# Kernel optimization log

Measured on AMD Instinct MI355X. Metric: run time of the kernel, lower is better.

Reference implementation:

```python
import jax, jax.numpy as jnp
import numpy as np

MIN_PS = 4
MAX_PS = 16


def _enforce(mb):
    # mb: (L,) bool candidate boundaries (merge_signal < 0.7-quantile)
    # Faithful re-implementation of _enforce_patch_size_constraints:
    # walk boundaries left->right, skip segments < MIN_PS (start not advanced),
    # accept otherwise, and insert ceil(ps/MAX_PS)-1 evenly spaced splits for
    # oversized segments. seq_len-1 is always appended as a candidate.
    L = mb.shape[0]
    pos = jnp.arange(L, dtype=jnp.int32)
    cand = mb | (pos == L - 1)

    def fwd_step(start, inp):
        p, is_c = inp
        ps = p - start
        acc = is_c & (ps >= MIN_PS)
        k = jnp.where(acc, (ps + MAX_PS - 1) // MAX_PS, jnp.int32(1))
        sz = jnp.maximum(jnp.where(acc, ps // k, jnp.int32(1)), 1)
        new_start = jnp.where(acc, p, start)
        return new_start, (acc, start, sz, k)

    _, (acc, seg_start, sz, k) = jax.lax.scan(fwd_step, jnp.int32(0), (pos, cand))

    # Reverse scan: propagate each accepted boundary's (start, split_size, num_splits)
    # back to the interior positions of its segment so splits can be placed in parallel.
    def rev_step(carry, inp):
        a, s, z, kk = inp
        cs, cz, ck, cv = carry
        out = (cs, cz, ck, cv)
        ncarry = (jnp.where(a, s, cs), jnp.where(a, z, cz), jnp.where(a, kk, ck), cv | a)
        return ncarry, out

    init = (jnp.int32(0), jnp.int32(1), jnp.int32(1), jnp.bool_(False))
    _, (fs, fz, fk, fv) = jax.lax.scan(rev_step, init, (acc, seg_start, sz, k), reverse=True)
    r = pos - fs
    j = r // fz
    split = fv & (r > 0) & (r % fz == 0) & (j >= 1) & (j <= fk - 1)
    return acc | split


def reference(x, attention_mask, W1, b1, W2, b2, Wc, bc, Wb1, bb1, Wb2, bb2):
    B, L, D = x.shape
    # content scorer: Linear -> ReLU -> Linear -> Sigmoid
    content = jax.nn.sigmoid(jax.nn.relu(x @ W1 + b1) @ W2 + b2)[..., 0]  # (B, L)
    # grouped Conv1d(d, d//2, k=3, pad=1, groups=d//4)
    xc = jnp.transpose(x, (0, 2, 1))  # (B, D, L)
    pf = jax.lax.conv_general_dilated(xc, Wc, (1,), ((1, 1),),
                                      feature_group_count=D // 4,
                                      dimension_numbers=('NCH', 'OIH', 'NCH'))
    pf = jnp.transpose(pf + bc[None, :, None], (0, 2, 1))  # (B, L, D//2)
    comb = jnp.concatenate([x, pf], axis=-1)
    bscore = jax.nn.sigmoid(jax.nn.relu(comb @ Wb1 + bb1) @ Wb2 + bb2)[..., 0]  # (B, L)
    signal = content * (1.0 - bscore) * attention_mask
    thr = jnp.quantile(signal, 0.7, axis=1, keepdims=True)
    mb = signal < thr
    new_b = jax.vmap(_enforce)(mb)  # (B, L) bool, new_b[:,0] is always False

    # segment id per token = inclusive cumsum of boundaries
    seg = jnp.cumsum(new_b.astype(jnp.int32), axis=1)
    seg_flat = (seg + jnp.arange(B, dtype=jnp.int32)[:, None] * L).reshape(-1)
    NS = B * L
    xm = x * attention_mask[..., None]
    e = jnp.sum(xm * xm, axis=-1).reshape(-1)  # softmax logits = ||token||^2
    m = jax.ops.segment_max(e, seg_flat, num_segments=NS)
    w = jnp.exp(e - m[seg_flat])
    denom = jax.ops.segment_sum(w, seg_flat, num_segments=NS)
    wn = w / denom[seg_flat]
    merged = jax.ops.segment_sum(xm.reshape(-1, D) * wn[:, None], seg_flat,
                                 num_segments=NS).reshape(B, L, D)
    # segment_boundaries: 1 for every segment except the first, zero padding
    n_last = seg[:, -1]
    p = jnp.arange(L)
    seg_bounds = ((p[None, :] >= 1) & (p[None, :] <= n_last[:, None])).astype(jnp.float32)
    return merged, seg_bounds


def setup_inputs() -> dict:
    key = jax.random.key(0)
    B, L, D = 4, 8192, 512
    ks = jax.random.split(key, 8)
    s = 0.02
    return {
        'x': jax.random.normal(ks[0], (B, L, D), jnp.float32),
        'attention_mask': jnp.ones((B, L), jnp.float32),
        'W1': jax.random.normal(ks[1], (D, D // 4), jnp.float32) * s,
        'b1': jnp.zeros((D // 4,), jnp.float32),
        'W2': jax.random.normal(ks[2], (D // 4, 1), jnp.float32) * s,
        'b2': jnp.zeros((1,), jnp.float32),
        'Wc': jax.random.normal(ks[3], (D // 2, 4, 3), jnp.float32) * s,
        'bc': jnp.zeros((D // 2,), jnp.float32),
        'Wb1': jax.random.normal(ks[4], (D + D // 2, D // 4), jnp.float32) * s,
        'bb1': jnp.zeros((D // 4,), jnp.float32),
        'Wb2': jax.random.normal(ks[5], (D // 4, 1), jnp.float32) * s,
        'bb2': jnp.zeros((1,), jnp.float32),
    }
```

## Files before the change

### kernel.cpp

```cpp
#include <hip/hip_runtime.h>
#include <math.h>

#define B_  4
#define L_  8192
#define D_  512
#define BL_ (B_*L_)
#define TOK 32
#define XS  36
#define KC  32
#define NCH (D_/KC)

__global__ __launch_bounds__(256, 4) void k_signal(
    const float* __restrict__ x, const float* __restrict__ mask,
    const float* __restrict__ W1, const float* __restrict__ b1,
    const float* __restrict__ W2, const float* __restrict__ b2,
    const float* __restrict__ Wc, const float* __restrict__ bc,
    const float* __restrict__ Wb1, const float* __restrict__ bb1,
    const float* __restrict__ Wb2, const float* __restrict__ bb2,
    float* __restrict__ signal, float* __restrict__ e)
{
  __shared__ float xt[KC][XS];
  __shared__ float pf[16][XS];

  const int t   = threadIdx.x;
  const int blk = blockIdx.x;
  const int b   = blk >> 8;
  const int l0  = (blk & 255) * TOK;
  const float* xb = x + (size_t)b * L_ * D_;

  const int jq = t & 31, tw = t >> 5;
  const int j0 = jq << 2, tok0 = tw << 2;

  const int stok = t >> 3, skk = t & 7;
  const int oo_c  = t >> 4;
  const int tokq  = t & 15;
  const int cb_c  = (oo_c >> 1) << 2;
  const int tok0c = tokq << 1;

  float a1[4][4], a2[4][4];
#pragma unroll
  for (int i = 0; i < 4; ++i)
#pragma unroll
    for (int j = 0; j < 4; ++j) { a1[i][j] = 0.f; a2[i][j] = 0.f; }
  float esacc = 0.f;

  for (int c = 0; c < NCH; ++c) {
    const int kc = c << 5;
    __syncthreads();

    {
      const float4 v = *reinterpret_cast<const float4*>(
          xb + (size_t)(l0 + stok) * D_ + kc + (skk << 2));
      esacc = fmaf(v.x, v.x, esacc); esacc = fmaf(v.y, v.y, esacc);
      esacc = fmaf(v.z, v.z, esacc); esacc = fmaf(v.w, v.w, esacc);
      const int r = skk << 2;
      xt[r + 0][stok] = v.x; xt[r + 1][stok] = v.y;
      xt[r + 2][stok] = v.z; xt[r + 3][stok] = v.w;
    }
    if (t < 16) {
      const int hh = t >> 3, kk = t & 7;
      const int l = hh ? (l0 + TOK) : (l0 - 1);
      float4 v = make_float4(0.f, 0.f, 0.f, 0.f);
      if (l >= 0 && l < L_)
        v = *reinterpret_cast<const float4*>(xb + (size_t)l * D_ + kc + (kk << 2));
      const int r = kk << 2, col = TOK + hh;
      xt[r + 0][col] = v.x; xt[r + 1][col] = v.y;
      xt[r + 2][col] = v.z; xt[r + 3][col] = v.w;
    }
    __syncthreads();

    {
      const int o = (c << 4) + oo_c;
      const float* wcp = Wc + o * 12;
      const float bco = bc[o];
      float acc0 = bco, acc1 = bco;
      const int tm1 = (tok0c == 0) ? TOK : tok0c - 1;
      const int tp2 = (tok0c == TOK - 2) ? TOK + 1 : tok0c + 2;
#pragma unroll
      for (int i = 0; i < 4; ++i) {
        const float w0 = wcp[i * 3 + 0], w1 = wcp[i * 3 + 1], w2 = wcp[i * 3 + 2];
        const float* row = &xt[cb_c + i][0];
        const float v0 = row[tm1], v1 = row[tok0c], v2 = row[tok0c + 1],
                    v3 = row[tp2];
        acc0 = fmaf(v2, w2, fmaf(v1, w1, fmaf(v0, w0, acc0)));
        acc1 = fmaf(v3, w2, fmaf(v2, w1, fmaf(v1, w0, acc1)));
      }
      pf[oo_c][tok0c]     = acc0;
      pf[oo_c][tok0c + 1] = acc1;
    }

    {
      const float* w1p = W1  + (size_t)kc * 128 + j0;
      const float* wbp = Wb1 + (size_t)kc * 128 + j0;
#pragma unroll 2
      for (int k = 0; k < KC; ++k) {
        const float4 w1 = *reinterpret_cast<const float4*>(w1p + (size_t)k * 128);
        const float4 wb = *reinterpret_cast<const float4*>(wbp + (size_t)k * 128);
        const float4 xv4 = *reinterpret_cast<const float4*>(&xt[k][tok0]);
        const float xv[4] = {xv4.x, xv4.y, xv4.z, xv4.w};
#pragma unroll
        for (int i = 0; i < 4; ++i) {
          a1[i][0] = fmaf(xv[i], w1.x, a1[i][0]);
          a1[i][1] = fmaf(xv[i], w1.y, a1[i][1]);
          a1[i][2] = fmaf(xv[i], w1.z, a1[i][2]);
          a1[i][3] = fmaf(xv[i], w1.w, a1[i][3]);
          a2[i][0] = fmaf(xv[i], wb.x, a2[i][0]);
          a2[i][1] = fmaf(xv[i], wb.y, a2[i][1]);
          a2[i][2] = fmaf(xv[i], wb.z, a2[i][2]);
          a2[i][3] = fmaf(xv[i], wb.w, a2[i][3]);
        }
      }
    }
    __syncthreads();

    {
      const float* wpp = Wb1 + (size_t)(512 + (c << 4)) * 128 + j0;
#pragma unroll 2
      for (int oo = 0; oo < 16; ++oo) {
        const float4 wp = *reinterpret_cast<const float4*>(wpp + (size_t)oo * 128);
        const float4 pv4 = *reinterpret_cast<const float4*>(&pf[oo][tok0]);
        const float pv[4] = {pv4.x, pv4.y, pv4.z, pv4.w};
#pragma unroll
        for (int i = 0; i < 4; ++i) {
          a2[i][0] = fmaf(pv[i], wp.x, a2[i][0]);
          a2[i][1] = fmaf(pv[i], wp.y, a2[i][1]);
          a2[i][2] = fmaf(pv[i], wp.z, a2[i][2]);
          a2[i][3] = fmaf(pv[i], wp.w, a2[i][3]);
        }
      }
    }
  }

  {
    float b1v[4], w2v[4], bbv[4], wv2[4];
#pragma unroll
    for (int jj = 0; jj < 4; ++jj) {
      b1v[jj] = b1[j0 + jj];  w2v[jj] = W2[j0 + jj];
      bbv[jj] = bb1[j0 + jj]; wv2[jj] = Wb2[j0 + jj];
    }
    const float bias2 = b2[0], biasb2 = bb2[0];
#pragma unroll
    for (int i = 0; i < 4; ++i) {
      float p1 = 0.f, p2 = 0.f;
#pragma unroll
      for (int jj = 0; jj < 4; ++jj) {
        const float h1 = a1[i][jj] + b1v[jj];
        if (h1 > 0.f) p1 = fmaf(h1, w2v[jj], p1);
        const float h2 = a2[i][jj] + bbv[jj];
        if (h2 > 0.f) p2 = fmaf(h2, wv2[jj], p2);
      }
#pragma unroll
      for (int off = 1; off < 32; off <<= 1) {
        p1 += __shfl_xor(p1, off, 64);
        p2 += __shfl_xor(p2, off, 64);
      }
      if (jq == 0) {
        const int gi = b * L_ + l0 + tok0 + i;
        const float content = 1.f / (1.f + expf(-(p1 + bias2)));
        const float bscore  = 1.f / (1.f + expf(-(p2 + biasb2)));
        signal[gi] = content * (1.f - bscore) * mask[gi];
      }
    }
  }

  {
    float es = esacc;
    es += __shfl_xor(es, 1, 64);
    es += __shfl_xor(es, 2, 64);
    es += __shfl_xor(es, 4, 64);
    if ((t & 7) == 0) {
      const int gi = b * L_ + l0 + stok;
      const float m = mask[gi];
      e[gi] = m * m * es;
    }
  }
}

__device__ __forceinline__ int chain_sim(unsigned long long w, int from) {
  int last = -1;
  while (from < 64) {
    const unsigned long long m = w & (~0ull << from);
    if (m == 0ull) break;
    const int p = __ffsll(m) - 1;
    last = p;
    from = p + 4;
  }
  return last;
}

__global__ __launch_bounds__(1024) void k_select(
    const float* __restrict__ signal,
    int* __restrict__ starts, int* __restrict__ nlast, float* __restrict__ bounds)
{
  __shared__ unsigned int bins[4][256];
  __shared__ unsigned int sel_prefix;
  __shared__ int sel_rank;
  __shared__ float sh_thr;
  __shared__ unsigned int wmin[16];
  __shared__ int wcnt[16];
  __shared__ unsigned long long cw[128];
  __shared__ unsigned char nb[L_];
  __shared__ signed char tbl[128][4];
  __shared__ int st_in[128];
  __shared__ int tsum[256];
  __shared__ int offs[257];

  const int b = blockIdx.x, t = threadIdx.x;
  const int wv = t >> 6, lane = t & 63;
  const float* s = signal + b * L_;

  float val[8];
  unsigned int key[8];
#pragma unroll
  for (int i = 0; i < 8; ++i) {
    val[i] = s[(i << 10) + t];
    const unsigned int u = __float_as_uint(val[i]);
    key[i] = (u & 0x80000000u) ? ~u : (u | 0x80000000u);
  }

  if (t == 0) { sel_prefix = 0u; sel_rank = 5733; }
  __syncthreads();
  for (int round = 0; round < 4; ++round) {
    reinterpret_cast<unsigned int*>(bins)[t] = 0u;
    __syncthreads();
    const unsigned int pre = sel_prefix;
    const int shift = 24 - 8 * round;
#pragma unroll
    for (int i = 0; i < 8; ++i) {
      if (round == 0 || (key[i] >> (shift + 8)) == pre)
        atomicAdd(&bins[t >> 8][(key[i] >> shift) & 255u], 1u);
    }
    __syncthreads();
    if (t < 256)
      bins[0][t] = bins[0][t] + bins[1][t] + bins[2][t] + bins[3][t];
    __syncthreads();
    if (t < 64) {
      const unsigned int c0 = bins[0][(t << 2) + 0], c1 = bins[0][(t << 2) + 1];
      const unsigned int c2 = bins[0][(t << 2) + 2], c3 = bins[0][(t << 2) + 3];
      const unsigned int lsum = c0 + c1 + c2 + c3;
      unsigned int run = lsum;
#pragma unroll
      for (int off = 1; off < 64; off <<= 1) {
        const unsigned int v = __shfl_up(run, off, 64);
        if (t >= off) run += v;
      }
      const int r = sel_rank;
      if (r >= (int)(run - lsum) && r < (int)run) {
        int rr = r - (int)(run - lsum);
        unsigned int cbin;
        if (rr < (int)c0) { cbin = 0; }
        else if (rr < (int)(c0 + c1)) { cbin = 1; rr -= (int)c0; }
        else if (rr < (int)(c0 + c1 + c2)) { cbin = 2; rr -= (int)(c0 + c1); }
        else { cbin = 3; rr -= (int)(c0 + c1 + c2); }
        sel_rank = rr;
        sel_prefix = (pre << 8) | ((unsigned int)(t << 2) | cbin);
      }
    }
    __syncthreads();
  }
  const unsigned int k0 = sel_prefix;

  {
    int cle = 0;
    unsigned int mgt = 0xFFFFFFFFu;
#pragma unroll
    for (int i = 0; i < 8; ++i) {
      if (key[i] <= k0) ++cle;
      else mgt = min(mgt, key[i]);
    }
#pragma unroll
    for (int off = 1; off < 64; off <<= 1) {
      cle += __shfl_xor(cle, off, 64);
      mgt = min(mgt, (unsigned int)__shfl_xor((int)mgt, off, 64));
    }
    if (lane == 0) { wcnt[wv] = cle; wmin[wv] = mgt; }
    __syncthreads();
    if (t == 0) {
      int C = 0; unsigned int M = 0xFFFFFFFFu;
      for (int g = 0; g < 16; ++g) { C += wcnt[g]; M = min(M, wmin[g]); }
      const unsigned int k1 = (C >= 5735) ? k0 : M;
      const unsigned int u0 = (k0 & 0x80000000u) ? (k0 & 0x7fffffffu) : ~k0;
      const unsigned int u1 = (k1 & 0x80000000u) ? (k1 & 0x7fffffffu) : ~k1;
      const float v0 = __uint_as_float(u0);
      const float v1 = __uint_as_float(u1);
      const float g = 0.7f * 8191.0f - 5733.0f;
      sh_thr = v0 + g * (v1 - v0);
    }
    __syncthreads();
  }
  const float thr = sh_thr;

#pragma unroll
  for (int i = 0; i < 8; ++i) {
    const unsigned long long m = __ballot(val[i] < thr);
    if (lane == 0) cw[(i << 4) + wv] = m;
  }
  {
    const int base = t << 3;
#pragma unroll
    for (int i = 0; i < 8; ++i) nb[base + i] = 0;
  }
  __syncthreads();
  if (t == 0) cw[127] |= (1ull << 63);
  __syncthreads();

  if (t < 512) {
    const int blk = t >> 2, cls = t & 3;
    tbl[blk][cls] = (signed char)chain_sim(cw[blk], cls);
  }
  __syncthreads();

  if (t == 0) {
    int st = 0;
    for (int blk = 0; blk < 128; ++blk) {
      const int bs = blk << 6;
      st_in[blk] = st;
      int pl;
      if (blk == 0) {
        pl = chain_sim(cw[0], 4);
      } else {
        int off = st + 4 - bs;
        if (off < 0) off = 0;
        pl = tbl[blk][off];
      }
      if (pl >= 0) st = bs + pl;
    }
  }
  __syncthreads();

  if (t < 128) {
    const int bs = t << 6;
    const unsigned long long w = cw[t];
    int st = st_in[t];
    int from = st + 4 - bs;
    if (from < 0) from = 0;
    while (from < 64) {
      const unsigned long long m = w & (~0ull << from);
      if (m == 0ull) break;
      const int p_rel = __ffsll(m) - 1;
      const int p = bs + p_rel;
      nb[p] = 1;
      const int ps = p - st;
      const int k = (ps + 15) >> 4;
      if (k > 1) {
        int sz = ps / k; if (sz < 1) sz = 1;
        for (int j = 1; j < k; ++j) nb[st + j * sz] = 1;
      }
      st = p;
      from = p_rel + 4;
    }
  }
  __syncthreads();

  if (t < 256) {
    const int base = t << 5;
    int ls = 0;
    for (int i = 0; i < 32; ++i) ls += nb[base + i];
    tsum[t] = ls;
  }
  __syncthreads();
  if (t == 0) {
    int r = 0;
    for (int i = 0; i < 256; ++i) { offs[i] = r; r += tsum[i]; }
    offs[256] = r;
  }
  __syncthreads();
  if (t < 256) {
    const int base = t << 5;
    int run = offs[t];
    for (int i = 0; i < 32; ++i) {
      run += nb[base + i];
      if (nb[base + i]) starts[b * L_ + run] = base + i;
    }
  }
  if (t == 0) { starts[b * L_ + 0] = 0; nlast[b] = offs[256]; }
  __syncthreads();
  const int total = offs[256];
  for (int i = t; i < L_; i += 1024)
    bounds[b * L_ + i] = (i >= 1 && i <= total) ? 1.0f : 0.0f;
}

__global__ __launch_bounds__(64) void k_merge(const float* __restrict__ x,
    const float* __restrict__ mask, const float* __restrict__ e,
    const int* __restrict__ starts, const int* __restrict__ nlast,
    float* __restrict__ merged)
{
  const int idx = blockIdx.x;
  const int b   = idx >> 13;
  const int sid = idx & (L_ - 1);
  const int n = nlast[b];
  const int lane = threadIdx.x;
  const int c0 = lane << 3;
  float* o = merged + (size_t)(b * L_ + sid) * D_ + c0;
  if (sid > n) {
    const float4 z = make_float4(0.f, 0.f, 0.f, 0.f);
    reinterpret_cast<float4*>(o)[0] = z;
    reinterpret_cast<float4*>(o)[1] = z;
    return;
  }
  const int t0 = starts[b * L_ + sid];
  const int t1 = (sid < n) ? starts[b * L_ + sid + 1] : L_;
  const float* eb = e + b * L_;

  float mx = -INFINITY;
  for (int p = t0; p < t1; ++p) mx = fmaxf(mx, eb[p]);
  float den = 0.f;
  for (int p = t0; p < t1; ++p) den += expf(eb[p] - mx);

  float acc[8] = {0,0,0,0,0,0,0,0};
  for (int p = t0; p < t1; ++p) {
    const float wn = expf(eb[p] - mx) / den;
    const float sc = wn * mask[b * L_ + p];
    const float* xr = x + ((size_t)(b * L_ + p)) * D_ + c0;
    const float4 u0 = reinterpret_cast<const float4*>(xr)[0];
    const float4 u1 = reinterpret_cast<const float4*>(xr)[1];
    acc[0] = fmaf(sc, u0.x, acc[0]); acc[1] = fmaf(sc, u0.y, acc[1]);
    acc[2] = fmaf(sc, u0.z, acc[2]); acc[3] = fmaf(sc, u0.w, acc[3]);
    acc[4] = fmaf(sc, u1.x, acc[4]); acc[5] = fmaf(sc, u1.y, acc[5]);
    acc[6] = fmaf(sc, u1.z, acc[6]); acc[7] = fmaf(sc, u1.w, acc[7]);
  }
  reinterpret_cast<float4*>(o)[0] = make_float4(acc[0], acc[1], acc[2], acc[3]);
  reinterpret_cast<float4*>(o)[1] = make_float4(acc[4], acc[5], acc[6], acc[7]);
}

extern "C" void kernel_launch(void* const* d_in, const int* in_sizes, int n_in,
                              void* d_out, int out_size, void* d_ws, size_t ws_size,
                              hipStream_t stream) {
  (void)in_sizes; (void)n_in; (void)out_size; (void)ws_size;
  const float* x    = (const float*)d_in[0];
  const float* mask = (const float*)d_in[1];
  const float* W1   = (const float*)d_in[2];
  const float* b1   = (const float*)d_in[3];
  const float* W2   = (const float*)d_in[4];
  const float* b2   = (const float*)d_in[5];
  const float* Wc   = (const float*)d_in[6];
  const float* bc   = (const float*)d_in[7];
  const float* Wb1  = (const float*)d_in[8];
  const float* bb1  = (const float*)d_in[9];
  const float* Wb2  = (const float*)d_in[10];
  const float* bb2  = (const float*)d_in[11];

  float* merged = (float*)d_out;
  float* bounds = (float*)d_out + (size_t)BL_ * D_;

  char* ws = (char*)d_ws;
  float* signal = (float*)(ws);
  float* e      = (float*)(ws + (size_t)BL_ * 4);
  int*   starts = (int*)  (ws + (size_t)BL_ * 8);
  int*   nlast  = (int*)  (ws + (size_t)BL_ * 12);

  k_signal<<<BL_ / TOK, 256, 0, stream>>>(x, mask, W1, b1, W2, b2, Wc, bc,
                                          Wb1, bb1, Wb2, bb2, signal, e);
  k_select<<<B_, 1024, 0, stream>>>(signal, starts, nlast, bounds);
  k_merge<<<BL_, 64, 0, stream>>>(x, mask, e, starts, nlast, merged);
}
```

Measured before the change: 341.0 us.

## Stage weight tiles in shared memory and halve the K chunk

Each K chunk of W1, Wb1 and the conv-feature rows of Wb1 is now loaded cooperatively into shared memory, so the inner FMA loops read weights from LDS instead of issuing per-thread global loads. The chunk size drops from 32 to 16 to keep LDS use bounded, and the x-tile load and conv thread mapping change to match: each thread now computes one conv output instead of two. This doubles the number of chunk iterations and barriers, and adds about 18KB of LDS per block, which may limit occupancy.

After: 316.1 us. 1.08x faster.

```diff
diff --git a/kernel.cpp b/kernel.cpp
--- a/kernel.cpp
+++ b/kernel.cpp
@@ -7,7 +7,7 @@
 #define BL_ (B_*L_)
 #define TOK 32
 #define XS  36
-#define KC  32
+#define KC  16
 #define NCH (D_/KC)
 
 __global__ __launch_bounds__(256, 4) void k_signal(
@@ -19,8 +19,11 @@
     const float* __restrict__ Wb2, const float* __restrict__ bb2,
     float* __restrict__ signal, float* __restrict__ e)
 {
+  __shared__ float ws1[KC][128];
+  __shared__ float wsb[KC][128];
+  __shared__ float wsp[8][128];
   __shared__ float xt[KC][XS];
-  __shared__ float pf[16][XS];
+  __shared__ float pf[8][XS];
 
   const int t   = threadIdx.x;
   const int blk = blockIdx.x;
@@ -31,11 +34,10 @@
   const int jq = t & 31, tw = t >> 5;
   const int j0 = jq << 2, tok0 = tw << 2;
 
-  const int stok = t >> 3, skk = t & 7;
-  const int oo_c  = t >> 4;
-  const int tokq  = t & 15;
+  const int stok = t >> 2, skk = t & 3;
+  const int oo_c  = t >> 5;
+  const int tokc  = t & 31;
   const int cb_c  = (oo_c >> 1) << 2;
-  const int tok0c = tokq << 1;
 
   float a1[4][4], a2[4][4];
 #pragma unroll
@@ -45,10 +47,31 @@
   float esacc = 0.f;
 
   for (int c = 0; c < NCH; ++c) {
-    const int kc = c << 5;
+    const int kc = c << 4;
     __syncthreads();
 
     {
+      const int row = t >> 5, c4 = (t & 31) << 2;
+      {
+        const float4 v0 = *reinterpret_cast<const float4*>(W1 + (size_t)(kc + row) * 128 + c4);
+        const float4 v1 = *reinterpret_cast<const float4*>(W1 + (size_t)(kc + 8 + row) * 128 + c4);
+        *reinterpret_cast<float4*>(&ws1[row][c4]) = v0;
+        *reinterpret_cast<float4*>(&ws1[8 + row][c4]) = v1;
+      }
+      {
+        const float4 v0 = *reinterpret_cast<const float4*>(Wb1 + (size_t)(kc + row) * 128 + c4);
+        const float4 v1 = *reinterpret_cast<const float4*>(Wb1 + (size_t)(kc + 8 + row) * 128 + c4);
+        *reinterpret_cast<float4*>(&wsb[row][c4]) = v0;
+        *reinterpret_cast<float4*>(&wsb[8 + row][c4]) = v1;
+      }
+      {
+        const float4 v0 = *reinterpret_cast<const float4*>(
+            Wb1 + (size_t)(512 + (c << 3) + row) * 128 + c4);
+        if (row < 8) *reinterpret_cast<float4*>(&wsp[row][c4]) = v0;
+      }
+    }
+
+    if (t < 128) {
       const float4 v = *reinterpret_cast<const float4*>(
           xb + (size_t)(l0 + stok) * D_ + kc + (skk << 2));
       esacc = fmaf(v.x, v.x, esacc); esacc = fmaf(v.y, v.y, esacc);
@@ -56,9 +79,9 @@
       const int r = skk << 2;
       xt[r + 0][stok] = v.x; xt[r + 1][stok] = v.y;
       xt[r + 2][stok] = v.z; xt[r + 3][stok] = v.w;
-    }
-    if (t < 16) {
-      const int hh = t >> 3, kk = t & 7;
+    } else if (t < 136) {
+      const int q = t - 128;
+      const int hh = q >> 2, kk = q & 3;
       const int l = hh ? (l0 + TOK) : (l0 - 1);
       float4 v = make_float4(0.f, 0.f, 0.f, 0.f);
       if (l >= 0 && l < L_)
@@ -70,63 +93,57 @@
     __syncthreads();
 
     {
-      const int o = (c << 4) + oo_c;
+      const int o = (c << 3) + oo_c;
       const float* wcp = Wc + o * 12;
-      const float bco = bc[o];
-      float acc0 = bco, acc1 = bco;
-      const int tm1 = (tok0c == 0) ? TOK : tok0c - 1;
-      const int tp2 = (tok0c == TOK - 2) ? TOK + 1 : tok0c + 2;
+      const float4 wq0 = *reinterpret_cast<const float4*>(wcp);
+      const float4 wq1 = *reinterpret_cast<const float4*>(wcp + 4);
+      const float4 wq2 = *reinterpret_cast<const float4*>(wcp + 8);
+      const float wc12[12] = {wq0.x, wq0.y, wq0.z, wq0.w, wq1.x, wq1.y,
+                              wq1.z, wq1.w, wq2.x, wq2.y, wq2.z, wq2.w};
+      float acc = bc[o];
+      const int tm1 = (tokc == 0) ? TOK : tokc - 1;
+      const int tp1 = (tokc == TOK - 1) ? TOK + 1 : tokc + 1;
 #pragma unroll
       for (int i = 0; i < 4; ++i) {
-        const float w0 = wcp[i * 3 + 0], w1 = wcp[i * 3 + 1], w2 = wcp[i * 3 + 2];
         const float* row = &xt[cb_c + i][0];
-        const float v0 = row[tm1], v1 = row[tok0c], v2 = row[tok0c + 1],
-                    v3 = row[tp2];
-        acc0 = fmaf(v2, w2, fmaf(v1, w1, fmaf(v0, w0, acc0)));
-        acc1 = fmaf(v3, w2, fmaf(v2, w1, fmaf(v1, w0, acc1)));
-      }
-      pf[oo_c][tok0c]     = acc0;
-      pf[oo_c][tok0c + 1] = acc1;
-    }
-
-    {
-      const float* w1p = W1  + (size_t)kc * 128 + j0;
-      const float* wbp = Wb1 + (size_t)kc * 128 + j0;
-#pragma unroll 2
-      for (int k = 0; k < KC; ++k) {
-        const float4 w1 = *reinterpret_cast<const float4*>(w1p + (size_t)k * 128);
-        const float4 wb = *reinterpret_cast<const float4*>(wbp + (size_t)k * 128);
-        const float4 xv4 = *reinterpret_cast<const float4*>(&xt[k][tok0]);
-        const float xv[4] = {xv4.x, xv4.y, xv4.z, xv4.w};
-#pragma unroll
-        for (int i = 0; i < 4; ++i) {
-          a1[i][0] = fmaf(xv[i], w1.x, a1[i][0]);
-          a1[i][1] = fmaf(xv[i], w1.y, a1[i][1]);
-          a1[i][2] = fmaf(xv[i], w1.z, a1[i][2]);
-          a1[i][3] = fmaf(xv[i], w1.w, a1[i][3]);
-          a2[i][0] = fmaf(xv[i], wb.x, a2[i][0]);
-          a2[i][1] = fmaf(xv[i], wb.y, a2[i][1]);
-          a2[i][2] = fmaf(xv[i], wb.z, a2[i][2]);
-          a2[i][3] = fmaf(xv[i], wb.w, a2[i][3]);
-        }
-      }
-    }
-    __syncthreads();
-
-    {
-      const float* wpp = Wb1 + (size_t)(512 + (c << 4)) * 128 + j0;
-#pragma unroll 2
-      for (int oo = 0; oo < 16; ++oo) {
-        const float4 wp = *reinterpret_cast<const float4*>(wpp + (size_t)oo * 128);
-        const float4 pv4 = *reinterpret_cast<const float4*>(&pf[oo][tok0]);
-        const float pv[4] = {pv4.x, pv4.y, pv4.z, pv4.w};
-#pragma unroll
-        for (int i = 0; i < 4; ++i) {
-          a2[i][0] = fmaf(pv[i], wp.x, a2[i][0]);
-          a2[i][1] = fmaf(pv[i], wp.y, a2[i][1]);
-          a2[i][2] = fmaf(pv[i], wp.z, a2[i][2]);
-          a2[i][3] = fmaf(pv[i], wp.w, a2[i][3]);
-        }
+        acc = fmaf(row[tm1],  wc12[i * 3 + 0], acc);
+        acc = fmaf(row[tokc], wc12[i * 3 + 1], acc);
+        acc = fmaf(row[tp1],  wc12[i * 3 + 2], acc);
+      }
+      pf[oo_c][tokc] = acc;
+    }
+
+#pragma unroll 4
+    for (int k = 0; k < KC; ++k) {
+      const float4 w1 = *reinterpret_cast<const float4*>(&ws1[k][j0]);
+      const float4 wb = *reinterpret_cast<const float4*>(&wsb[k][j0]);
+      const float4 xv = *reinterpret_cast<const float4*>(&xt[k][tok0]);
+      const float xs4[4] = {xv.x, xv.y, xv.z, xv.w};
+#pragma unroll
+      for (int i = 0; i < 4; ++i) {
+        a1[i][0] = fmaf(xs4[i], w1.x, a1[i][0]);
+        a1[i][1] = fmaf(xs4[i], w1.y, a1[i][1]);
+        a1[i][2] = fmaf(xs4[i], w1.z, a1[i][2]);
+        a1[i][3] = fmaf(xs4[i], w1.w, a1[i][3]);
+        a2[i][0] = fmaf(xs4[i], wb.x, a2[i][0]);
+        a2[i][1] = fmaf(xs4[i], wb.y, a2[i][1]);
+        a2[i][2] = fmaf(xs4[i], wb.z, a2[i][2]);
+        a2[i][3] = fmaf(xs4[i], wb.w, a2[i][3]);
+      }
+    }
+    __syncthreads();
+
+#pragma unroll 4
+    for (int oo = 0; oo < 8; ++oo) {
+      const float4 wp = *reinterpret_cast<const float4*>(&wsp[oo][j0]);
+      const float4 pv = *reinterpret_cast<const float4*>(&pf[oo][tok0]);
+      const float ps4[4] = {pv.x, pv.y, pv.z, pv.w};
+#pragma unroll
+      for (int i = 0; i < 4; ++i) {
+        a2[i][0] = fmaf(ps4[i], wp.x, a2[i][0]);
+        a2[i][1] = fmaf(ps4[i], wp.y, a2[i][1]);
+        a2[i][2] = fmaf(ps4[i], wp.z, a2[i][2]);
+        a2[i][3] = fmaf(ps4[i], wp.w, a2[i][3]);
       }
     }
   }
@@ -163,12 +180,11 @@
     }
   }
 
-  {
+  if (t < 128) {
     float es = esacc;
     es += __shfl_xor(es, 1, 64);
     es += __shfl_xor(es, 2, 64);
-    es += __shfl_xor(es, 4, 64);
-    if ((t & 7) == 0) {
+    if (skk == 0) {
       const int gi = b * L_ + l0 + stok;
       const float m = mask[gi];
       e[gi] = m * m * es;
```
